# Performance work log

Hardware: AMD Instinct MI355X
Metric: run time of the kernel (lower is better)

Reference implementation:

```python
import jax, jax.numpy as jnp
import numpy as np

DK = 64
DROPOUT_P = 0.1


def setup_inputs() -> dict:
    key = jax.random.key(0)
    kq, kk, kv, km = jax.random.split(key, 4)
    B, S, D = 16, 2048, 64
    q = jax.random.normal(kq, (B, S, D), dtype=jnp.float32)
    k = jax.random.normal(kk, (B, S, D), dtype=jnp.float32)
    v = jax.random.normal(kv, (B, S, D), dtype=jnp.float32)
    attn_mask = jax.random.randint(km, (S, S), 0, 2, dtype=jnp.int32)
    return {"q": q, "k": k, "v": v, "attn_mask": attn_mask}


def reference(q, k, v, attn_mask):
    # q = q / sqrt(dk)
    qs = q * (1.0 / np.sqrt(DK)).astype(np.float32)
    # dots: [B, S_q, S_k]
    dots = jnp.einsum("bqd,bkd->bqk", qs, k)
    # mask: 0 -> -inf, 1 -> 0 (additive)
    add_mask = jnp.where(attn_mask == 0, -jnp.inf, 0.0).astype(dots.dtype)
    dots = dots + add_mask  # broadcast [S,S] over batch
    attn = jax.nn.softmax(dots, axis=-1)
    # inverted dropout, train mode, fixed key for determinism
    keep = jax.random.bernoulli(jax.random.key(42), 1.0 - DROPOUT_P, attn.shape)
    attn = jnp.where(keep, attn * (1.0 / (1.0 - DROPOUT_P)), 0.0)
    out = jnp.einsum("bqk,bkd->bqd", attn, v)
    return out
```

## Files before the change

kernel.cpp:

```cpp
#include <hip/hip_runtime.h>

#define BATCH 16
#define SEQ   2048
#define DIM   64
#define NTHREADS 256
#define NROWS    (BATCH * SEQ)
#define OUTELEMS (NROWS * DIM)

typedef short bf16x8 __attribute__((ext_vector_type(8)));
typedef float f32x4 __attribute__((ext_vector_type(4)));

__device__ __forceinline__ int ldsoff(int row) {
  return row * 72 + 16 * (row >> 2);
}
#define LDS_SZ (64 * 72 + 16 * 16)

__device__ __forceinline__ unsigned tf_bits(unsigned f) {
  unsigned x0 = 0u;
  unsigned x1 = f;
  const unsigned ks1 = 42u;
  const unsigned ks2 = 0x1BD11BDAu ^ 42u;
  x1 += ks1;
#define TF_R(r) { x0 += x1; x1 = __builtin_amdgcn_alignbit(x1, x1, 32u - (r)); x1 ^= x0; }
  TF_R(13) TF_R(15) TF_R(26) TF_R(6)
  x0 += ks1; x1 += ks2 + 1u;
  TF_R(17) TF_R(29) TF_R(16) TF_R(24)
  x0 += ks2; x1 += 2u;
  TF_R(13) TF_R(15) TF_R(26) TF_R(6)
  x1 += ks1 + 3u;
  TF_R(17) TF_R(29) TF_R(16) TF_R(24)
  x0 += ks1; x1 += ks2 + 4u;
  TF_R(13) TF_R(15) TF_R(26) TF_R(6)
  x0 += ks2; x1 += 5u;
#undef TF_R
  return x0 ^ x1;
}
#define KEEP_THRESH 0xE6666600u

__device__ __forceinline__ unsigned pack_bf16x2(float lo, float hi) {
  const unsigned l = (__float_as_uint(lo) + 0x8000u) >> 16;
  const unsigned h = (__float_as_uint(hi) + 0x8000u) & 0xFFFF0000u;
  return h | l;
}
__device__ __forceinline__ unsigned pack_trunc(float lo, float hi) {
  return __builtin_amdgcn_perm(__float_as_uint(hi), __float_as_uint(lo), 0x07060302u);
}

#define WS_KF 0
#define WS_VF 1048576

__global__ __launch_bounds__(NTHREADS)
void convert_kv(const float* __restrict__ k, const float* __restrict__ v,
                unsigned* __restrict__ ws) {
  const unsigned gid = blockIdx.x * NTHREADS + threadIdx.x;
  const unsigned e = gid & 262143u;
  const int lane = e & 63;
  const int ks = (e >> 6) & 1, nt = (e >> 7) & 3, kt = (e >> 9) & 31, b = e >> 14;
  const int tx = lane & 15, quad = lane >> 4;
  uint4 wout;
  if (gid < 262144u) {
    const float* src = k + ((size_t)b * SEQ + kt * 64 + 4 * tx + nt) * DIM
                         + ks * 32 + quad * 8;
    const float4 f0 = *(const float4*)src;
    const float4 f1 = *(const float4*)(src + 4);
    wout.x = pack_bf16x2(f0.x, f0.y); wout.y = pack_bf16x2(f0.z, f0.w);
    wout.z = pack_bf16x2(f1.x, f1.y); wout.w = pack_bf16x2(f1.z, f1.w);
    *(uint4*)(ws + WS_KF + (size_t)e * 4) = wout;
  } else {
    const float* src = v + ((size_t)b * SEQ + kt * 64 + ks * 32 + quad * 8) * DIM
                         + nt * 16 + tx;
    const float a0 = src[0 * DIM], a1 = src[1 * DIM], a2 = src[2 * DIM], a3 = src[3 * DIM];
    const float a4 = src[4 * DIM], a5 = src[5 * DIM], a6 = src[6 * DIM], a7 = src[7 * DIM];
    wout.x = pack_bf16x2(a0, a1); wout.y = pack_bf16x2(a2, a3);
    wout.z = pack_bf16x2(a4, a5); wout.w = pack_bf16x2(a6, a7);
    *(uint4*)(ws + WS_VF + (size_t)e * 4) = wout;
  }
}

__global__ __launch_bounds__(NTHREADS, 2)
void attn_fwd(const float* __restrict__ q, const unsigned* __restrict__ ws,
              const int* __restrict__ mask, float* __restrict__ out) {
  __shared__ unsigned short PS[LDS_SZ];

  const int t    = threadIdx.x;
  const int w    = t >> 6;
  const int lane = t & 63;
  const int tx   = lane & 15;
  const int quad = lane >> 4;

  const int bb = blockIdx.x >> 5;
  const int q0 = (blockIdx.x & 31) * 64;
  const int qw = q0 + 16 * w;

  const float qscale = 0.125f * 1.44269504088896340736f;

  bf16x8 aq[2];
  {
    const float* qr = q + ((size_t)bb * SEQ + qw + tx) * DIM + quad * 8;
#pragma unroll
    for (int ks = 0; ks < 2; ++ks) {
      const float4 f0 = *(const float4*)(qr + ks * 32);
      const float4 f1 = *(const float4*)(qr + ks * 32 + 4);
      union { unsigned u[4]; bf16x8 v; } a;
      a.u[0] = pack_bf16x2(f0.x * qscale, f0.y * qscale);
      a.u[1] = pack_bf16x2(f0.z * qscale, f0.w * qscale);
      a.u[2] = pack_bf16x2(f1.x * qscale, f1.y * qscale);
      a.u[3] = pack_bf16x2(f1.z * qscale, f1.w * qscale);
      aq[ks] = a.v;
    }
  }

  float lrun[4] = {0.f, 0.f, 0.f, 0.f};
  f32x4 oacc[4];
#pragma unroll
  for (int nt = 0; nt < 4; ++nt) oacc[nt] = (f32x4){0.f, 0.f, 0.f, 0.f};

  const unsigned* kfb = ws + WS_KF + (size_t)(bb * 32) * 2048 + (size_t)lane * 4;
  const unsigned* vfb = ws + WS_VF + (size_t)(bb * 32) * 2048 + (size_t)lane * 4;
  const int* mbase = mask + (size_t)(qw + quad * 4) * SEQ + 4 * tx;
  const unsigned fbase0 = (unsigned)(bb * SEQ + qw + quad * 4) * (unsigned)SEQ
                          + (unsigned)(4 * tx);

  bf16x8 vfA[4][2], vfB[4][2];

#define RNG_PWRITE(kt_, qk_)                                                   \
  {                                                                            \
    const unsigned fb = fbase0 + (unsigned)((kt_) * 64);                       \
    _Pragma("unroll")                                                          \
    for (int reg = 0; reg < 4; ++reg) {                                        \
      const int* mreg = (const int*)&mv[reg];                                  \
      float pd[4];                                                             \
      float ls = 0.0f;                                                         \
      _Pragma("unroll")                                                        \
      for (int nt = 0; nt < 4; ++nt) {                                         \
        const float s = mreg[nt] ? qk_[nt][reg] : -1e30f;                      \
        const float e = __builtin_amdgcn_exp2f(s);                             \
        ls += e;                                                               \
        const unsigned bits = tf_bits(fb + (unsigned)(reg * SEQ) + (unsigned)nt); \
        pd[nt] = (bits < KEEP_THRESH) ? e : 0.0f;                              \
      }                                                                        \
      lrun[reg] += ls;                                                         \
      uint2 pw;                                                                \
      pw.x = pack_trunc(pd[0], pd[1]);                                         \
      pw.y = pack_trunc(pd[2], pd[3]);                                         \
      *(uint2*)&PS[ldsoff(16 * w + quad * 4 + reg) + 4 * tx] = pw;             \
    }                                                                          \
  }

  {
    const unsigned* kfp = kfb;
    const unsigned* vfp = vfb;
    bf16x8 kf[4][2];
#pragma unroll
    for (int nt = 0; nt < 4; ++nt)
#pragma unroll
      for (int ks = 0; ks < 2; ++ks) {
        kf[nt][ks]  = *(const bf16x8*)(kfp + (nt * 2 + ks) * 256);
        vfA[nt][ks] = *(const bf16x8*)(vfp + (nt * 2 + ks) * 256);
      }
    int4 mv[4];
#pragma unroll
    for (int reg = 0; reg < 4; ++reg)
      mv[reg] = *(const int4*)(mbase + (size_t)reg * SEQ);
    f32x4 qk[4];
#pragma unroll
    for (int nt = 0; nt < 4; ++nt) {
      f32x4 c = (f32x4){0.f, 0.f, 0.f, 0.f};
#pragma unroll
      for (int ks = 0; ks < 2; ++ks)
        c = __builtin_amdgcn_mfma_f32_16x16x32_bf16(aq[ks], kf[nt][ks], c, 0, 0, 0);
      qk[nt] = c;
    }
    RNG_PWRITE(0, qk)
  }

#define BODY(kt_, prevV, curV)                                                 \
  {                                                                            \
    const unsigned* kfp = kfb + (size_t)(kt_) * 2048;                          \
    const unsigned* vfp = vfb + (size_t)(kt_) * 2048;                          \
    bf16x8 kf[4][2];                                                           \
    _Pragma("unroll")                                                          \
    for (int nt = 0; nt < 4; ++nt)                                             \
      _Pragma("unroll")                                                        \
      for (int ks = 0; ks < 2; ++ks) {                                         \
        kf[nt][ks]   = *(const bf16x8*)(kfp + (nt * 2 + ks) * 256);            \
        curV[nt][ks] = *(const bf16x8*)(vfp + (nt * 2 + ks) * 256);            \
      }                                                                        \
    int4 mv[4];                                                                \
    _Pragma("unroll")                                                          \
    for (int reg = 0; reg < 4; ++reg)                                          \
      mv[reg] = *(const int4*)(mbase + (size_t)reg * SEQ + (kt_) * 64);        \
    _Pragma("unroll")                                                          \
    for (int ks = 0; ks < 2; ++ks) {                                           \
      const bf16x8 ap = *(const bf16x8*)&PS[ldsoff(16 * w + tx) + ks * 32 + quad * 8]; \
      _Pragma("unroll")                                                        \
      for (int nt = 0; nt < 4; ++nt)                                           \
        oacc[nt] = __builtin_amdgcn_mfma_f32_16x16x32_bf16(ap, prevV[nt][ks],  \
                                                           oacc[nt], 0, 0, 0); \
    }                                                                          \
    f32x4 qk[4];                                                               \
    _Pragma("unroll")                                                          \
    for (int nt = 0; nt < 4; ++nt) {                                           \
      f32x4 c = (f32x4){0.f, 0.f, 0.f, 0.f};                                   \
      _Pragma("unroll")                                                        \
      for (int ks = 0; ks < 2; ++ks)                                           \
        c = __builtin_amdgcn_mfma_f32_16x16x32_bf16(aq[ks], kf[nt][ks], c, 0, 0, 0); \
      qk[nt] = c;                                                              \
    }                                                                          \
    RNG_PWRITE(kt_, qk)                                                        \
  }

#pragma unroll 1
  for (int kt = 1; kt < 31; kt += 2) {
    BODY(kt, vfA, vfB)
    BODY(kt + 1, vfB, vfA)
  }
  BODY(31, vfA, vfB)

#pragma unroll
  for (int ks = 0; ks < 2; ++ks) {
    const bf16x8 ap = *(const bf16x8*)&PS[ldsoff(16 * w + tx) + ks * 32 + quad * 8];
#pragma unroll
    for (int nt = 0; nt < 4; ++nt)
      oacc[nt] = __builtin_amdgcn_mfma_f32_16x16x32_bf16(ap, vfB[nt][ks], oacc[nt], 0, 0, 0);
  }

  float linv[4];
#pragma unroll
  for (int reg = 0; reg < 4; ++reg) {
    float ls = lrun[reg];
    ls += __shfl_xor(ls, 1);
    ls += __shfl_xor(ls, 2);
    ls += __shfl_xor(ls, 4);
    ls += __shfl_xor(ls, 8);
    linv[reg] = (1.0f / 0.9f) / ls;
  }
  float* ob = out + ((size_t)bb * SEQ + qw) * DIM;
#pragma unroll
  for (int nt = 0; nt < 4; ++nt)
#pragma unroll
    for (int reg = 0; reg < 4; ++reg)
      ob[(size_t)(quad * 4 + reg) * DIM + nt * 16 + tx] = oacc[nt][reg] * linv[reg];
}

extern "C" void kernel_launch(void* const* d_in, const int* in_sizes, int n_in,
                              void* d_out, int out_size, void* d_ws, size_t ws_size,
                              hipStream_t stream) {
  const float* q = (const float*)d_in[0];
  const float* k = (const float*)d_in[1];
  const float* v = (const float*)d_in[2];
  const int* mask = (const int*)d_in[3];
  float* out = (float*)d_out;
  unsigned* ws = (unsigned*)d_ws;

  hipLaunchKernelGGL(convert_kv, dim3(2048), dim3(NTHREADS), 0, stream, k, v, ws);
  hipLaunchKernelGGL(attn_fwd, dim3(512), dim3(NTHREADS), 0, stream,
                     q, ws, mask, out);
}
```

Measured before the change: 232.1 us.

## Precompute dropout keep bits and mask bitmaps in prep kernel

Moves the Threefry dropout RNG out of the attention inner loop into the preprocessing kernel, which produces packed keep bitmaps via ballot. The int32 mask is likewise compressed to a bitmap, so the main kernel reads one 64-bit word each for keep and mask per tile instead of four int4 loads and sixteen hash evaluations. Per element, the work is the same amount of RNG, now done in a separate fully parallel pass. The cost is an extra 64MB-class bitmap write and read through the workspace plus a larger prep launch.

```diff
diff --git a/kernel.cpp b/kernel.cpp
--- a/kernel.cpp
+++ b/kernel.cpp
@@ -4,11 +4,10 @@
 #define SEQ   2048
 #define DIM   64
 #define NTHREADS 256
-#define NROWS    (BATCH * SEQ)
-#define OUTELEMS (NROWS * DIM)
 
 typedef short bf16x8 __attribute__((ext_vector_type(8)));
 typedef float f32x4 __attribute__((ext_vector_type(4)));
+typedef unsigned long long u64;
 
 __device__ __forceinline__ int ldsoff(int row) {
   return row * 72 + 16 * (row >> 2);
@@ -46,17 +45,63 @@
   return __builtin_amdgcn_perm(__float_as_uint(hi), __float_as_uint(lo), 0x07060302u);
 }
 
-#define WS_KF 0
-#define WS_VF 1048576
-
-__global__ __launch_bounds__(NTHREADS)
-void convert_kv(const float* __restrict__ k, const float* __restrict__ v,
-                unsigned* __restrict__ ws) {
-  const unsigned gid = blockIdx.x * NTHREADS + threadIdx.x;
+#define WS_KF   0
+#define WS_VF   1048576
+#define WS_KEEP 2097152
+#define WS_MB   4194304
+
+__global__ __launch_bounds__(NTHREADS, 8)
+void convert_kv_rng(const float* __restrict__ k, const float* __restrict__ v,
+                    const int* __restrict__ mask, unsigned* __restrict__ ws) {
+  const int t = threadIdx.x;
+  const int lane = t & 63;
+  const int tx = lane & 15, quad = lane >> 4;
+
+  if (blockIdx.x >= 4096) {
+    const int wv = ((int)blockIdx.x - 4096) * 4 + (t >> 6);
+#pragma unroll 1
+    for (int i = 0; i < 64; i += 2) {
+      const int m0 = wv * 64 + i;
+      u64 bb[2];
+#pragma unroll
+      for (int j = 0; j < 2; ++j) {
+        const int m = m0 + j;
+        const int qq = 4 * (m >> 7) + quad;
+        const int kk = 16 * (m & 127) + tx;
+        bb[j] = __ballot(mask[(size_t)qq * SEQ + kk] != 0);
+      }
+      if (lane == 0) {
+        uint4 st;
+        st.x = (unsigned)bb[0]; st.y = (unsigned)(bb[0] >> 32);
+        st.z = (unsigned)bb[1]; st.w = (unsigned)(bb[1] >> 32);
+        *(uint4*)(ws + WS_MB + (size_t)m0 * 2) = st;
+      }
+    }
+    return;
+  }
+
+  if (blockIdx.x & 1) {
+    const int w = ((int)(blockIdx.x >> 1) << 2) + (t >> 6);
+    unsigned f = (unsigned)(w * 4 + quad) * 2048u + (unsigned)tx;
+    unsigned* wp = ws + WS_KEEP + (size_t)w * 256;
+#pragma unroll 1
+    for (int i = 0; i < 128; i += 2) {
+      const u64 b0 = __ballot(tf_bits(f) < KEEP_THRESH);
+      const u64 b1 = __ballot(tf_bits(f + 16u) < KEEP_THRESH);
+      f += 32u;
+      if (lane == 0) {
+        uint4 st;
+        st.x = (unsigned)b0; st.y = (unsigned)(b0 >> 32);
+        st.z = (unsigned)b1; st.w = (unsigned)(b1 >> 32);
+        *(uint4*)(wp + i * 2) = st;
+      }
+    }
+    return;
+  }
+
+  const unsigned gid = (unsigned)(blockIdx.x >> 1) * NTHREADS + (unsigned)t;
   const unsigned e = gid & 262143u;
-  const int lane = e & 63;
   const int ks = (e >> 6) & 1, nt = (e >> 7) & 3, kt = (e >> 9) & 31, b = e >> 14;
-  const int tx = lane & 15, quad = lane >> 4;
   uint4 wout;
   if (gid < 262144u) {
     const float* src = k + ((size_t)b * SEQ + kt * 64 + 4 * tx + nt) * DIM
@@ -79,7 +124,7 @@
 
 __global__ __launch_bounds__(NTHREADS, 2)
 void attn_fwd(const float* __restrict__ q, const unsigned* __restrict__ ws,
-              const int* __restrict__ mask, float* __restrict__ out) {
+              float* __restrict__ out) {
   __shared__ unsigned short PS[LDS_SZ];
 
   const int t    = threadIdx.x;
@@ -117,27 +162,33 @@
 
   const unsigned* kfb = ws + WS_KF + (size_t)(bb * 32) * 2048 + (size_t)lane * 4;
   const unsigned* vfb = ws + WS_VF + (size_t)(bb * 32) * 2048 + (size_t)lane * 4;
-  const int* mbase = mask + (size_t)(qw + quad * 4) * SEQ + 4 * tx;
-  const unsigned fbase0 = (unsigned)(bb * SEQ + qw + quad * 4) * (unsigned)SEQ
-                          + (unsigned)(4 * tx);
+  const u64* keepb = (const u64*)(ws + WS_KEEP)
+                     + (size_t)(bb * 512 + (qw >> 2) + quad) * 128 + (tx >> 2);
+  const u64* maskb = (const u64*)(ws + WS_MB)
+                     + (size_t)((qw >> 2) + quad) * 128 + (tx >> 2);
+  const int ksh = 4 * (tx & 3);
 
   bf16x8 vfA[4][2], vfB[4][2];
 
-#define RNG_PWRITE(kt_, qk_)                                                   \
+#define RNG_PWRITE(qk_, kw_, mw_)                                              \
   {                                                                            \
-    const unsigned fb = fbase0 + (unsigned)((kt_) * 64);                       \
+    const u64 kws = (kw_) >> ksh;                                              \
+    const u64 mws = (mw_) >> ksh;                                              \
+    const unsigned klo = (unsigned)kws, khi = (unsigned)(kws >> 32);           \
+    const unsigned mlo = (unsigned)mws, mhi = (unsigned)(mws >> 32);           \
     _Pragma("unroll")                                                          \
     for (int reg = 0; reg < 4; ++reg) {                                        \
-      const int* mreg = (const int*)&mv[reg];                                  \
+      const unsigned knib = ((reg & 2) ? khi : klo) >> ((reg & 1) * 16);       \
+      const unsigned mnib = ((reg & 2) ? mhi : mlo) >> ((reg & 1) * 16);       \
+      const unsigned cnib = knib & mnib;                                       \
       float pd[4];                                                             \
       float ls = 0.0f;                                                         \
       _Pragma("unroll")                                                        \
       for (int nt = 0; nt < 4; ++nt) {                                         \
-        const float s = mreg[nt] ? qk_[nt][reg] : -1e30f;                      \
+        const float s = (mnib & (1u << nt)) ? qk_[nt][reg] : -1e30f;           \
         const float e = __builtin_amdgcn_exp2f(s);                             \
         ls += e;                                                               \
-        const unsigned bits = tf_bits(fb + (unsigned)(reg * SEQ) + (unsigned)nt); \
-        pd[nt] = (bits < KEEP_THRESH) ? e : 0.0f;                              \
+        pd[nt] = (cnib & (1u << nt)) ? e : 0.0f;                               \
       }                                                                        \
       lrun[reg] += ls;                                                         \
       uint2 pw;                                                                \
@@ -158,10 +209,8 @@
         kf[nt][ks]  = *(const bf16x8*)(kfp + (nt * 2 + ks) * 256);
         vfA[nt][ks] = *(const bf16x8*)(vfp + (nt * 2 + ks) * 256);
       }
-    int4 mv[4];
-#pragma unroll
-    for (int reg = 0; reg < 4; ++reg)
-      mv[reg] = *(const int4*)(mbase + (size_t)reg * SEQ);
+    const u64 kwv = keepb[0];
+    const u64 mwv = maskb[0];
     f32x4 qk[4];
 #pragma unroll
     for (int nt = 0; nt < 4; ++nt) {
@@ -171,7 +220,7 @@
         c = __builtin_amdgcn_mfma_f32_16x16x32_bf16(aq[ks], kf[nt][ks], c, 0, 0, 0);
       qk[nt] = c;
     }
-    RNG_PWRITE(0, qk)
+    RNG_PWRITE(qk, kwv, mwv)
   }
 
 #define BODY(kt_, prevV, curV)                                                 \
@@ -186,10 +235,8 @@
         kf[nt][ks]   = *(const bf16x8*)(kfp + (nt * 2 + ks) * 256);            \
         curV[nt][ks] = *(const bf16x8*)(vfp + (nt * 2 + ks) * 256);            \
       }                                                                        \
-    int4 mv[4];                                                                \
-    _Pragma("unroll")                                                          \
-    for (int reg = 0; reg < 4; ++reg)                                          \
-      mv[reg] = *(const int4*)(mbase + (size_t)reg * SEQ + (kt_) * 64);        \
+    const u64 kwv = keepb[(kt_) * 4];                                          \
+    const u64 mwv = maskb[(kt_) * 4];                                          \
     _Pragma("unroll")                                                          \
     for (int ks = 0; ks < 2; ++ks) {                                           \
       const bf16x8 ap = *(const bf16x8*)&PS[ldsoff(16 * w + tx) + ks * 32 + quad * 8]; \
@@ -207,7 +254,7 @@
         c = __builtin_amdgcn_mfma_f32_16x16x32_bf16(aq[ks], kf[nt][ks], c, 0, 0, 0); \
       qk[nt] = c;                                                              \
     }                                                                          \
-    RNG_PWRITE(kt_, qk)                                                        \
+    RNG_PWRITE(qk, kwv, mwv)                                                   \
   }
 
 #pragma unroll 1
@@ -253,7 +300,8 @@
   float* out = (float*)d_out;
   unsigned* ws = (unsigned*)d_ws;
 
-  hipLaunchKernelGGL(convert_kv, dim3(2048), dim3(NTHREADS), 0, stream, k, v, ws);
+  hipLaunchKernelGGL(convert_kv_rng, dim3(4352), dim3(NTHREADS), 0, stream,
+                     k, v, mask, ws);
   hipLaunchKernelGGL(attn_fwd, dim3(512), dim3(NTHREADS), 0, stream,
-                     q, ws, mask, out);
-}
+                     q, ws, out);
+}
```

Measured after the change: 440.7 us. 89.9% more time.
